# Optimization experiments

Measured on AMD Instinct MI355X. Metric: run time of the kernel, lower is better.

The kernel has to match this reference:

```python
import jax, jax.numpy as jnp
import numpy as np

N, E = 10000, 160000
MUL0, MUL1, MUL2 = 64, 32, 16
DIM = MUL0 + MUL1 * 3 + MUL2 * 5          # 240
LAT, CPL, NTYPE = 128, 128, 95
NGATE = MUL1 + MUL2                        # 48 gate scalars
NCH = MUL0 + MUL1 + MUL2                   # 112 irrep channels
AVG_NEI = 16.0

# scaling_indices: per-channel index repeated over each irrep's dim
SCALE_IDX = np.concatenate([
    np.arange(MUL0),
    np.repeat(np.arange(MUL0, MUL0 + MUL1), 3),
    np.repeat(np.arange(MUL0 + MUL1, NCH), 5),
])


def _split(x, n):
    s = x[:, :MUL0]
    v1 = x[:, MUL0:MUL0 + MUL1 * 3].reshape(n, MUL1, 3)
    v2 = x[:, MUL0 + MUL1 * 3:].reshape(n, MUL2, 5)
    return s, v1, v2


def setup_inputs() -> dict:
    key = jax.random.key(0)
    ks = iter(jax.random.split(key, 48))
    rn = lambda *s: jax.random.normal(next(ks), s, dtype=jnp.float32)
    return dict(
        node_features=rn(N, DIM), edge_features=rn(E, DIM),
        latents=rn(E, LAT), msg_cpl=rn(N, CPL),
        node_onehot=jax.random.uniform(next(ks), (N, NTYPE), dtype=jnp.float32),
        wigner_D1=rn(E, 3, 3), wigner_D2=rn(E, 5, 5),
        so2_W0=rn(2 * MUL0, MUL0 + NGATE) * 0.08, so2_W1=rn(2 * MUL1, MUL1) * 0.12,
        so2_W2=rn(2 * MUL2, MUL2) * 0.17, so2_Ws=rn(LAT, NCH + NGATE) * 0.08,
        env_W=rn(LAT, NCH) * 0.08,
        post_W0=rn(MUL0, MUL0) * 0.12, post_b0=rn(MUL0) * 0.01,
        post_W1=rn(MUL1, MUL1) * 0.17, post_W2=rn(MUL2, MUL2) * 0.25,
        res_W0=rn(MUL0, MUL0) * 0.12, res_b0=rn(MUL0) * 0.01,
        res_W1=rn(MUL1, MUL1) * 0.17, res_W2=rn(MUL2, MUL2) * 0.25,
        cpl_W1=rn(CPL, CPL) * 0.08, cpl_b1=rn(CPL) * 0.01,
        cpl_W2=rn(CPL, NCH) * 0.08, cpl_b2=rn(NCH) * 0.01,
        gs_W=rn(MUL0, CPL) * 0.12, gs_b=rn(CPL) * 0.01,
        msg_W1=rn(2 * CPL, CPL) * 0.06, msg_b1=rn(CPL) * 0.01,
        msg_W2=rn(CPL, CPL) * 0.08, msg_b2=rn(CPL) * 0.01,
        ln_g=jnp.ones(CPL, jnp.float32), ln_b=jnp.zeros(CPL, jnp.float32),
        oh_w0=rn(MUL0, NTYPE) * 0.1, oh_w1=rn(MUL1, NTYPE) * 0.1, oh_w2=rn(MUL2, NTYPE) * 0.1,
        edge_index=jax.random.randint(next(ks), (2, E), 0, N),
    )


def _forward(node_features, edge_features, latents, msg_cpl, node_onehot,
             wigner_D1, wigner_D2, so2_W0, so2_W1, so2_W2, so2_Ws, env_W,
             post_W0, post_b0, post_W1, post_W2, res_W0, res_b0, res_W1, res_W2,
             cpl_W1, cpl_b1, cpl_W2, cpl_b2, gs_W, gs_b,
             msg_W1, msg_b1, msg_W2, msg_b2, ln_g, ln_b,
             oh_w0, oh_w1, oh_w2, edge_index):
    src = edge_index[0]
    ns, nv1, nv2 = _split(node_features, N)
    es, ev1, ev2 = _split(edge_features, E)
    # gather node feats to edges, concat with edge feats (per-l blocks)
    s_in = jnp.concatenate([ns[src], es], axis=1)                 # [E,128]
    v1_in = jnp.concatenate([nv1[src], ev1], axis=1)              # [E,64,3]
    v2_in = jnp.concatenate([nv2[src], ev2], axis=1)              # [E,32,5]
    # rotate into per-edge frame (Wigner D)
    v1_r = jnp.einsum('eij,ecj->eci', wigner_D1, v1_in)
    v2_r = jnp.einsum('eij,ecj->eci', wigner_D2, v2_in)
    # SO2 linear: shared channel mixing + latent-conditioned per-channel scales
    sc = latents @ so2_Ws                                         # [E,160]
    s_m = (s_in @ so2_W0) * sc[:, :MUL0 + NGATE]
    v1_m = jnp.einsum('eci,co->eoi', v1_r, so2_W1) * sc[:, MUL0 + NGATE:MUL0 + NGATE + MUL1, None]
    v2_m = jnp.einsum('eci,co->eoi', v2_r, so2_W2) * sc[:, MUL0 + NGATE + MUL1:, None]
    # rotate back
    v1_m = jnp.einsum('eji,eci->ecj', wigner_D1, v1_m)
    v2_m = jnp.einsum('eji,eci->ecj', wigner_D2, v2_m)
    # Gate activation
    s_act = jax.nn.silu(s_m[:, :MUL0])
    gates = jax.nn.sigmoid(s_m[:, MUL0:])
    v1_g = v1_m * gates[:, :MUL1, None]
    v2_g = v2_m * gates[:, MUL1:, None]
    # lin_post (per-l linear, bias on scalars)
    s_p = s_act @ post_W0 + post_b0
    v1_p = jnp.einsum('eci,co->eoi', v1_g, post_W1)
    v2_p = jnp.einsum('eci,co->eoi', v2_g, post_W2)
    # env element-wise weighting from latents
    w = latents @ env_W                                           # [E,112]
    s_p = s_p * w[:, :MUL0]
    v1_p = v1_p * w[:, MUL0:MUL0 + MUL1, None]
    v2_p = v2_p * w[:, MUL0 + MUL1:, None]
    msg = jnp.concatenate([s_p, v1_p.reshape(E, -1), v2_p.reshape(E, -1)], axis=1)
    # scatter-reduce to nodes + neighbor normalization
    agg = jax.ops.segment_sum(msg, src, num_segments=N) * (AVG_NEI ** -0.5)
    # coupling coefficients (per-channel, expanded by scaling_indices)
    coeffs = jax.nn.silu(msg_cpl @ cpl_W1 + cpl_b1) @ cpl_W2 + cpl_b2
    new_nf = agg * coeffs[:, SCALE_IDX]
    # coupling-channel update
    scal = new_nf[:, :MUL0] @ gs_W + gs_b
    h = jnp.concatenate([scal, msg_cpl], axis=1)
    upd = jax.nn.silu(h @ msg_W1 + msg_b1) @ msg_W2 + msg_b2
    mc = msg_cpl + upd
    mu = mc.mean(-1, keepdims=True)
    var = mc.var(-1, keepdims=True)
    msg_cpl_out = (mc - mu) * jax.lax.rsqrt(var + 1e-5) * ln_g + ln_b
    # residual mix with fixed logit-0 coefficients
    c = jax.nn.sigmoid(jnp.float32(0.0))
    c_old = jax.lax.rsqrt(c * c + 1.0)
    c_new = c * c_old
    rs = ns @ res_W0 + res_b0
    rv1 = jnp.einsum('eci,co->eoi', nv1, res_W1)
    rv2 = jnp.einsum('eci,co->eoi', nv2, res_W2)
    res = jnp.concatenate([rs, rv1.reshape(N, -1), rv2.reshape(N, -1)], axis=1)
    nf = c_new * new_nf + c_old * res
    # layer one-hot tensor product ('uvu' with 95x0e)
    inv = 1.0 / np.sqrt(NTYPE).astype(np.float32)
    g0 = (node_onehot @ oh_w0.T) * inv
    g1 = (node_onehot @ oh_w1.T) * inv
    g2 = (node_onehot @ oh_w2.T) * inv
    os_, ov1, ov2 = _split(nf, N)
    oh = jnp.concatenate([os_ * g0, (ov1 * g1[:, :, None]).reshape(N, -1),
                          (ov2 * g2[:, :, None]).reshape(N, -1)], axis=1)
    return nf + oh, msg_cpl_out


def reference(node_features, edge_features, latents, msg_cpl, node_onehot,
              wigner_D1, wigner_D2, so2_W0, so2_W1, so2_W2, so2_Ws, env_W,
              post_W0, post_b0, post_W1, post_W2, res_W0, res_b0, res_W1, res_W2,
              cpl_W1, cpl_b1, cpl_W2, cpl_b2, gs_W, gs_b,
              msg_W1, msg_b1, msg_W2, msg_b2, ln_g, ln_b,
              oh_w0, oh_w1, oh_w2, edge_index):
    return _forward(node_features, edge_features, latents, msg_cpl, node_onehot,
                    wigner_D1, wigner_D2, so2_W0, so2_W1, so2_W2, so2_Ws, env_W,
                    post_W0, post_b0, post_W1, post_W2, res_W0, res_b0, res_W1, res_W2,
                    cpl_W1, cpl_b1, cpl_W2, cpl_b2, gs_W, gs_b,
                    msg_W1, msg_b1, msg_W2, msg_b2, ln_g, ln_b,
                    oh_w0, oh_w1, oh_w2, edge_index)
```

## Files before the change

kernel.cpp:

```cpp
#include <hip/hip_runtime.h>

#define NN   10000
#define NE   160000
#define DIM  240
#define EB   16
#define NPB  16

typedef __bf16 bf16x8 __attribute__((ext_vector_type(8)));
typedef __bf16 bf16x4 __attribute__((ext_vector_type(4)));
typedef float  f32x4  __attribute__((ext_vector_type(4)));

__device__ __forceinline__ float sigf(float x) { return 1.0f / (1.0f + __expf(-x)); }

#define OFF_WB1 0
#define OFF_WB2 34816
#define OFF_W1  49152
#define OFF_W2  51200
#define OFF_PW0 51712
#define OFF_PW1 55808
#define OFF_PW2 56832
#define OHT_BYTE_OFF 131072
#define CNT_BYTE_OFF 196608
#define ROW_BYTE_OFF 237568
#define CUR_BYTE_OFF 282624
#define EID_BYTE_OFF 327680

__global__ __launch_bounds__(256) void prep_kernel(
    const float* __restrict__ Ws, const float* __restrict__ We, const float* __restrict__ W0,
    const float* __restrict__ W1, const float* __restrict__ W2,
    const float* __restrict__ pW0, const float* __restrict__ pW1, const float* __restrict__ pW2,
    const float* __restrict__ w0g, const float* __restrict__ w1g, const float* __restrict__ w2g,
    __bf16* __restrict__ wsb, float* __restrict__ ohT,
    const int* __restrict__ src, int* __restrict__ cnt)
{
    if (blockIdx.x >= 56) {
        if (cnt) {
            int e = (blockIdx.x - 56) * 256 + threadIdx.x;
            if (e < NE) atomicAdd(&cnt[src[e]], 1);
        }
        return;
    }
    int tid = blockIdx.x * 256 + threadIdx.x;
    const int stride = 56 * 256;
    for (int idx = tid; idx < 17*4*512; idx += stride) {
        int j = idx & 7, lane = (idx >> 3) & 63, ks = (idx >> 9) & 3, nt = idx >> 11;
        int k = ks*32 + (lane >> 4)*8 + j, n = nt*16 + (lane & 15);
        float v = (n < 160) ? Ws[k*160 + n] : We[k*112 + (n - 160)];
        wsb[OFF_WB1 + idx] = (__bf16)v;
    }
    for (int idx = tid; idx < 7*4*512; idx += stride) {
        int j = idx & 7, lane = (idx >> 3) & 63, ks = (idx >> 9) & 3, nt = idx >> 11;
        int k = ks*32 + (lane >> 4)*8 + j, n = nt*16 + (lane & 15);
        wsb[OFF_WB2 + idx] = (__bf16)W0[k*112 + n];
    }
    for (int idx = tid; idx < 2*2*512; idx += stride) {
        int j = idx & 7, lane = (idx >> 3) & 63, ks = (idx >> 9) & 1, nt = idx >> 10;
        int k = ks*32 + (lane >> 4)*8 + j, n = nt*16 + (lane & 15);
        wsb[OFF_W1 + idx] = (__bf16)W1[k*32 + n];
    }
    for (int idx = tid; idx < 512; idx += stride) {
        int j = idx & 7, lane = (idx >> 3) & 63;
        int k = (lane >> 4)*8 + j, n = lane & 15;
        wsb[OFF_W2 + idx] = (__bf16)W2[k*16 + n];
    }
    for (int idx = tid; idx < 4*2*512; idx += stride) {
        int j = idx & 7, lane = (idx >> 3) & 63, ks = (idx >> 9) & 1, nt = idx >> 10;
        int k = ks*32 + (lane >> 4)*8 + j, n = nt*16 + (lane & 15);
        wsb[OFF_PW0 + idx] = (__bf16)pW0[k*64 + n];
    }
    for (int idx = tid; idx < 2*512; idx += stride) {
        int j = idx & 7, lane = (idx >> 3) & 63, nt = idx >> 9;
        int k = (lane >> 4)*8 + j, n = nt*16 + (lane & 15);
        wsb[OFF_PW1 + idx] = (__bf16)pW1[k*32 + n];
    }
    for (int idx = tid; idx < 512; idx += stride) {
        int j = idx & 7, lane = (idx >> 3) & 63;
        int k = (lane >> 4)*8 + j, n = lane & 15;
        wsb[OFF_PW2 + idx] = (k < 16) ? (__bf16)pW2[k*16 + n] : (__bf16)0.0f;
    }
    for (int idx = tid; idx < 96*112; idx += stride) {
        int k = idx / 112, n2 = idx - k*112;
        float v = 0.f;
        if (k < 95) {
            if (n2 < 64)      v = w0g[n2*95 + k];
            else if (n2 < 96) v = w1g[(n2-64)*95 + k];
            else              v = w2g[(n2-96)*95 + k];
        }
        ohT[idx] = v * 0.10259783521f;
    }
}

__global__ __launch_bounds__(256) void scan_kernel(const int* __restrict__ cnt,
                                                   int* __restrict__ rowptr, int* __restrict__ cur) {
    __shared__ int part[256];
    int t = threadIdx.x;
    int base = t * 40;
    int local[40];
    int s = 0;
    #pragma unroll
    for (int i = 0; i < 40; i++) {
        int idx = base + i;
        int v = (idx < NN) ? cnt[idx] : 0;
        local[i] = s; s += v;
    }
    part[t] = s;
    __syncthreads();
    for (int off = 1; off < 256; off <<= 1) {
        int v = (t >= off) ? part[t - off] : 0;
        __syncthreads();
        part[t] += v;
        __syncthreads();
    }
    int pre = (t > 0) ? part[t - 1] : 0;
    #pragma unroll
    for (int i = 0; i < 40; i++) {
        int idx = base + i;
        if (idx < NN) { int r = pre + local[i]; rowptr[idx] = r; cur[idx] = r; }
    }
    if (t == 255) rowptr[NN] = part[255];
}

__global__ __launch_bounds__(256) void fill_kernel(const int* __restrict__ src,
                                                   int* __restrict__ cur, int* __restrict__ eidl) {
    int e = blockIdx.x * 256 + threadIdx.x;
    if (e < NE) {
        int slot = atomicAdd(&cur[src[e]], 1);
        eidl[slot] = e;
    }
}

__global__ __launch_bounds__(256, 4) void edge_mfma_kernel(
    const float* __restrict__ nf, const float* __restrict__ ef,
    const float* __restrict__ latg, const float* __restrict__ D1g, const float* __restrict__ D2g,
    const float* __restrict__ pb0, const int* __restrict__ srcg,
    const int* __restrict__ eidl, const __bf16* __restrict__ wsb, float* agg)
{
    __shared__ __align__(16) unsigned char pool[40064];
    __bf16* Cb   = (__bf16*)(pool + 0);
    __bf16* aLat = (__bf16*)(pool + 12544);
    __bf16* aSin = (__bf16*)(pool + 16640);
    __bf16* v1m  = (__bf16*)(pool + 12544);
    __bf16* v2m  = (__bf16*)(pool + 16384);
    __bf16* mtile= (__bf16*)(pool + 12544);
    __bf16* vt1  = (__bf16*)(pool + 20736);
    __bf16* vt2  = (__bf16*)(pool + 27136);
    __bf16* aV1g = (__bf16*)(pool + 20736);
    __bf16* aV2g = (__bf16*)(pool + 23808);
    float*  d1s  = (float*)(pool + 32512);
    float*  d2s  = (float*)(pool + 33088);
    float*  gts  = (float*)(pool + 32512);
    __bf16* aSact= (__bf16*)(pool + 35648);
    float*  e1s  = (float*)(pool + 37696);
    float*  e2s  = (float*)(pool + 38272);
    int*    srcs = (int*)  (pool + 39872);
    int*    eids = (int*)  (pool + 39936);

    const int t    = threadIdx.x;
    const int wid  = t >> 6, lane = t & 63;
    const int e0   = blockIdx.x * EB;

    #define EIDX(e) (eidl ? eidl[e0 + (e)] : (e0 + (e)))

    bf16x8 bpre[8];
    {
        const __bf16* b0 = wsb + OFF_WB1 + wid*2048;
        const __bf16* b1 = wsb + OFF_WB1 + (wid + 4)*2048;
        #pragma unroll
        for (int ks = 0; ks < 4; ks++) {
            bpre[ks]     = *(const bf16x8*)(b0 + (ks*64 + lane)*8);
            bpre[4 + ks] = *(const bf16x8*)(b1 + (ks*64 + lane)*8);
        }
    }

    if (t < 16) { int ee = EIDX(t); eids[t] = ee; srcs[t] = srcg[ee]; }

    for (int idx = t; idx < 144; idx += 256) {
        int e = idx / 9; int ee = EIDX(e);
        d1s[idx] = D1g[(size_t)ee*9 + (idx - e*9)];
    }
    for (int idx = t; idx < 400; idx += 256) {
        int e = idx / 25; int ee = EIDX(e);
        d2s[idx] = D2g[(size_t)ee*25 + (idx - e*25)];
    }
    {
        int e = t >> 4, half = (t >> 3) & 1, cq = t & 7;
        int ee = EIDX(e);
        const float* base = half ? (ef + (size_t)ee*240 + 64 + cq*12)
                                 : (nf + (size_t)srcg[ee]*240 + 64 + cq*12);
        float4 f0 = *(const float4*)base;
        float4 f1 = *(const float4*)(base + 4);
        float4 f2 = *(const float4*)(base + 8);
        float f[12] = {f0.x,f0.y,f0.z,f0.w,f1.x,f1.y,f1.z,f1.w,f2.x,f2.y,f2.z,f2.w};
        int c = half*32 + cq*4;
        __bf16* dst = vt1 + e*200 + c;
        #pragma unroll
        for (int i = 0; i < 3; i++) {
            bf16x4 v = {(__bf16)f[i], (__bf16)f[3+i], (__bf16)f[6+i], (__bf16)f[9+i]};
            *(bf16x4*)(dst + i*64) = v;
        }
    }
    if (t < 128) {
        int e = t >> 3, half = (t >> 2) & 1, cq = t & 3;
        int ee = EIDX(e);
        const float* base = half ? (ef + (size_t)ee*240 + 160 + cq*20)
                                 : (nf + (size_t)srcg[ee]*240 + 160 + cq*20);
        float f[20];
        #pragma unroll
        for (int k = 0; k < 5; k++) {
            float4 q4 = *(const float4*)(base + k*4);
            f[4*k] = q4.x; f[4*k+1] = q4.y; f[4*k+2] = q4.z; f[4*k+3] = q4.w;
        }
        int c = half*16 + cq*4;
        __bf16* dst = vt2 + e*168 + c;
        #pragma unroll
        for (int z = 0; z < 5; z++) {
            bf16x4 v = {(__bf16)f[z], (__bf16)f[5+z], (__bf16)f[10+z], (__bf16)f[15+z]};
            *(bf16x4*)(dst + z*32) = v;
        }
    }
    {
        int ks = t >> 6, l2 = t & 63, e = l2 & 15;
        int k0 = ks*32 + (l2 >> 4)*8;
        int ee = EIDX(e);
        {
            const float4* p4 = (const float4*)(latg + (size_t)ee*128 + k0);
            float4 f0 = p4[0], f1 = p4[1];
            bf16x8 v;
            v[0]=(__bf16)f0.x; v[1]=(__bf16)f0.y; v[2]=(__bf16)f0.z; v[3]=(__bf16)f0.w;
            v[4]=(__bf16)f1.x; v[5]=(__bf16)f1.y; v[6]=(__bf16)f1.z; v[7]=(__bf16)f1.w;
            *(bf16x8*)(aLat + t*8) = v;
        }
        {
            const float* s2 = (k0 < 64) ? (nf + (size_t)srcg[ee]*240 + k0)
                                        : (ef + (size_t)ee*240 + (k0 - 64));
            const float4* p4 = (const float4*)s2;
            float4 f0 = p4[0], f1 = p4[1];
            bf16x8 v;
            v[0]=(__bf16)f0.x; v[1]=(__bf16)f0.y; v[2]=(__bf16)f0.z; v[3]=(__bf16)f0.w;
            v[4]=(__bf16)f1.x; v[5]=(__bf16)f1.y; v[6]=(__bf16)f1.z; v[7]=(__bf16)f1.w;
            *(bf16x8*)(aSin + t*8) = v;
        }
    }
    __syncthreads();

    {
        int col16 = lane & 15, ebase = (lane >> 4)*4;
        bf16x8 aL[4], aS[4];
        #pragma unroll
        for (int ks = 0; ks < 4; ks++) {
            aL[ks] = *(const bf16x8*)(aLat + (ks*64 + lane)*8);
            aS[ks] = *(const bf16x8*)(aSin + (ks*64 + lane)*8);
        }
        #pragma unroll
        for (int it = 0; it < 6; it++) {
            int nt = wid + it*4;
            bool isLat = nt < 17;
            const __bf16* bB = isLat ? (wsb + OFF_WB1 + nt*2048)
                                     : (wsb + OFF_WB2 + (nt - 17)*2048);
            f32x4 acc = {0.f, 0.f, 0.f, 0.f};
            #pragma unroll
            for (int ks = 0; ks < 4; ks++) {
                bf16x8 b;
                if (it < 2) b = bpre[it*4 + ks];
                else        b = *(const bf16x8*)(bB + (ks*64 + lane)*8);
                acc = __builtin_amdgcn_mfma_f32_16x16x32_bf16(isLat ? aL[ks] : aS[ks], b, acc, 0, 0, 0);
            }
            int col = (isLat ? nt*16 : 272 + (nt - 17)*16) + col16;
            #pragma unroll
            for (int r = 0; r < 4; r++) Cb[(ebase + r)*392 + col] = (__bf16)acc[r];
        }
    }
    for (int idx = t; idx < 544; idx += 256) {
        if (idx < 144) {
            int e = idx / 9, r = idx - e*9, i = r / 3, k = r - i*3;
            const float* d = d1s + e*9;
            e1s[idx] = d[i*3+0]*d[0*3+k] + d[i*3+1]*d[1*3+k] + d[i*3+2]*d[2*3+k];
        } else {
            int j = idx - 144;
            int e = j / 25, r = j - e*25, i = r / 5, k = r - i*5;
            const float* d = d2s + e*25;
            float a = 0.f;
            #pragma unroll
            for (int tt = 0; tt < 5; tt++) a += d[i*5+tt] * d[tt*5+k];
            e2s[j] = a;
        }
    }
    __syncthreads();

    {
        int col16 = lane & 15, er = lane & 15, q8 = (lane >> 4)*8, ebase = (lane >> 4)*4;
        for (int p = wid; p < 11; p += 4) {
            f32x4 acc = {0.f, 0.f, 0.f, 0.f};
            if (p < 6) {
                int i = p >> 1, nt = p & 1;
                #pragma unroll
                for (int ks = 0; ks < 2; ks++) {
                    bf16x8 a = *(const bf16x8*)(vt1 + er*200 + i*64 + ks*32 + q8);
                    bf16x8 b = *(const bf16x8*)(wsb + OFF_W1 + ((nt*2 + ks)*64 + lane)*8);
                    acc = __builtin_amdgcn_mfma_f32_16x16x32_bf16(a, b, acc, 0, 0, 0);
                }
                int col = nt*16 + col16;
                #pragma unroll
                for (int r = 0; r < 4; r++) v1m[(i*16 + ebase + r)*40 + col] = (__bf16)acc[r];
            } else {
                int i = p - 6;
                bf16x8 a = *(const bf16x8*)(vt2 + er*168 + i*32 + q8);
                bf16x8 b = *(const bf16x8*)(wsb + OFF_W2 + lane*8);
                acc = __builtin_amdgcn_mfma_f32_16x16x32_bf16(a, b, acc, 0, 0, 0);
                #pragma unroll
                for (int r = 0; r < 4; r++) v2m[(i*16 + ebase + r)*24 + col16] = (__bf16)acc[r];
            }
        }
    }
    if (t < 128) {
        int ks = t >> 6, l2 = t & 63, e = l2 & 15, o0 = ks*32 + (l2 >> 4)*8;
        bf16x8 v;
        #pragma unroll
        for (int j = 0; j < 8; j++) {
            int o = o0 + j;
            float x = (float)Cb[e*392 + 272 + o] * (float)Cb[e*392 + o];
            v[j] = (__bf16)(x * sigf(x));
        }
        *(bf16x8*)(aSact + t*8) = v;
    }
    for (int idx = t; idx < 768; idx += 256) {
        int e = idx / 48, o = idx - e*48;
        float x = (float)Cb[e*392 + 336 + o] * (float)Cb[e*392 + 64 + o];
        gts[e*49 + o] = sigf(x);
    }
    __syncthreads();

    for (int idx = t; idx < 512; idx += 256) {
        if (idx < 192) {
            int i = idx >> 6, l2 = idx & 63, e = l2 & 15, c0 = (l2 >> 4)*8;
            float z0 = e1s[e*9 + i*3], z1 = e1s[e*9 + i*3 + 1], z2 = e1s[e*9 + i*3 + 2];
            bf16x8 m0 = *(const bf16x8*)(v1m + (0*16 + e)*40 + c0);
            bf16x8 m1 = *(const bf16x8*)(v1m + (1*16 + e)*40 + c0);
            bf16x8 m2 = *(const bf16x8*)(v1m + (2*16 + e)*40 + c0);
            bf16x8 s8 = *(const bf16x8*)(Cb + e*392 + 112 + c0);
            bf16x8 v;
            #pragma unroll
            for (int j = 0; j < 8; j++) {
                float g = gts[e*49 + c0 + j];
                float a = z0*(float)m0[j] + z1*(float)m1[j] + z2*(float)m2[j];
                v[j] = (__bf16)(g * (float)s8[j] * a);
            }
            *(bf16x8*)(aV1g + idx*8) = v;
        } else {
            int idx2 = idx - 192;
            int i = idx2 >> 6, l2 = idx2 & 63, e = l2 & 15, c0 = (l2 >> 4)*8;
            bf16x8 v;
            if (c0 < 16) {
                const float* ee = e2s + e*25 + i*5;
                float z0 = ee[0], z1 = ee[1], z2 = ee[2], z3 = ee[3], z4 = ee[4];
                bf16x8 m0 = *(const bf16x8*)(v2m + (0*16 + e)*24 + c0);
                bf16x8 m1 = *(const bf16x8*)(v2m + (1*16 + e)*24 + c0);
                bf16x8 m2 = *(const bf16x8*)(v2m + (2*16 + e)*24 + c0);
                bf16x8 m3 = *(const bf16x8*)(v2m + (3*16 + e)*24 + c0);
                bf16x8 m4 = *(const bf16x8*)(v2m + (4*16 + e)*24 + c0);
                bf16x8 s8 = *(const bf16x8*)(Cb + e*392 + 144 + c0);
                #pragma unroll
                for (int j = 0; j < 8; j++) {
                    float g = gts[e*49 + 32 + c0 + j];
                    float a = z0*(float)m0[j] + z1*(float)m1[j] + z2*(float)m2[j]
                            + z3*(float)m3[j] + z4*(float)m4[j];
                    v[j] = (__bf16)(g * (float)s8[j] * a);
                }
            } else {
                #pragma unroll
                for (int j = 0; j < 8; j++) v[j] = (__bf16)0.0f;
            }
            *(bf16x8*)(aV2g + idx2*8) = v;
        }
    }
    __syncthreads();

    {
        int col16 = lane & 15, ebase = (lane >> 4)*4;
        for (int p = wid; p < 15; p += 4) {
            f32x4 acc = {0.f, 0.f, 0.f, 0.f};
            if (p < 4) {
                int nt = p;
                #pragma unroll
                for (int ks = 0; ks < 2; ks++) {
                    bf16x8 a = *(const bf16x8*)(aSact + (ks*64 + lane)*8);
                    bf16x8 b = *(const bf16x8*)(wsb + OFF_PW0 + ((nt*2 + ks)*64 + lane)*8);
                    acc = __builtin_amdgcn_mfma_f32_16x16x32_bf16(a, b, acc, 0, 0, 0);
                }
                int o = nt*16 + col16;
                float bias = pb0[o];
                #pragma unroll
                for (int r = 0; r < 4; r++) {
                    int e = ebase + r;
                    float val = (acc[r] + bias) * (float)Cb[e*392 + 160 + o];
                    if (eidl) mtile[e*248 + o] = (__bf16)val;
                    else      atomicAdd(agg + (size_t)srcs[e]*240 + o, val);
                }
            } else if (p < 10) {
                int q = p - 4, i = q >> 1, nt = q & 1;
                bf16x8 a = *(const bf16x8*)(aV1g + (i*64 + lane)*8);
                bf16x8 b = *(const bf16x8*)(wsb + OFF_PW1 + (nt*64 + lane)*8);
                acc = __builtin_amdgcn_mfma_f32_16x16x32_bf16(a, b, acc, 0, 0, 0);
                int o = nt*16 + col16;
                #pragma unroll
                for (int r = 0; r < 4; r++) {
                    int e = ebase + r;
                    float val = acc[r] * (float)Cb[e*392 + 224 + o];
                    if (eidl) mtile[e*248 + 64 + o*3 + i] = (__bf16)val;
                    else      atomicAdd(agg + (size_t)srcs[e]*240 + 64 + o*3 + i, val);
                }
            } else {
                int i = p - 10;
                bf16x8 a = *(const bf16x8*)(aV2g + (i*64 + lane)*8);
                bf16x8 b = *(const bf16x8*)(wsb + OFF_PW2 + lane*8);
                acc = __builtin_amdgcn_mfma_f32_16x16x32_bf16(a, b, acc, 0, 0, 0);
                #pragma unroll
                for (int r = 0; r < 4; r++) {
                    int e = ebase + r;
                    float val = acc[r] * (float)Cb[e*392 + 256 + col16];
                    if (eidl) mtile[e*248 + 160 + col16*5 + i] = (__bf16)val;
                    else      atomicAdd(agg + (size_t)srcs[e]*240 + 160 + col16*5 + i, val);
                }
            }
        }
    }

    if (eidl) {
        __syncthreads();
        if (t < 240) {
            float s = 0.f;
            int prev = srcs[0];
            #pragma unroll
            for (int e = 0; e < EB; e++) {
                int sn = srcs[e];
                if (sn != prev) {
                    atomicAdd(agg + (size_t)prev*240 + t, s);
                    s = 0.f; prev = sn;
                }
                s += (float)mtile[e*248 + t];
            }
            atomicAdd(agg + (size_t)prev*240 + t, s);
        }
    }
    #undef EIDX
}

__global__ __launch_bounds__(256, 2) void node_kernel(
    const float* __restrict__ nf, const float* __restrict__ mcplg,
    const float* __restrict__ ohg,
    const float* __restrict__ cW1, const float* __restrict__ cb1,
    const float* __restrict__ cW2, const float* __restrict__ cb2,
    const float* __restrict__ gsW, const float* __restrict__ gsb,
    const float* __restrict__ mW1, const float* __restrict__ mb1,
    const float* __restrict__ mW2, const float* __restrict__ mb2,
    const float* __restrict__ lng, const float* __restrict__ lnb,
    const float* __restrict__ rW0, const float* __restrict__ rb0,
    const float* __restrict__ rW1, const float* __restrict__ rW2,
    const float* __restrict__ ohT, float* out0, float* out1)
{
    __shared__ __align__(16) unsigned char pool[68608];
    float* mcp  = (float*)(pool + 0);
    float* ohv  = (float*)(pool + 8192);
    float* nsr  = (float*)(pool + 14336);
    float* anew = (float*)(pool + 29696);
    float* t12  = (float*)(pool + 45056);
    float* cfg  = (float*)(pool + 53248);
    float* scm  = (float*)(pool + 60416);

    const int t  = threadIdx.x;
    const int g  = t >> 7;
    const int o  = t & 127;
    const int nb = g * 8;
    const int n0 = blockIdx.x * NPB;

    for (int idx = t; idx < NPB * 128; idx += 256) {
        int n = idx >> 7, k = idx & 127;
        mcp[n*128 + k] = mcplg[(n0 + n) * 128 + k];
    }
    for (int idx = t; idx < NPB * 96; idx += 256) {
        int n = idx / 96, k = idx - n * 96;
        ohv[n*96 + k] = (k < 95) ? ohg[(n0 + n) * 95 + k] : 0.f;
    }
    for (int idx = t; idx < NPB * 240; idx += 256) {
        int n = idx / 240, k = idx - n * 240;
        nsr[n*240 + k]  = nf[(n0 + n) * DIM + k];
        anew[n*240 + k] = out0[(n0 + n) * DIM + k];
    }
    __syncthreads();

    {
        float a[8]; float b = cb1[o];
        #pragma unroll
        for (int i = 0; i < 8; i++) a[i] = b;
        #pragma unroll 2
        for (int k4 = 0; k4 < 32; k4++) {
            float w0 = cW1[(4*k4+0)*128 + o], w1 = cW1[(4*k4+1)*128 + o],
                  w2 = cW1[(4*k4+2)*128 + o], w3 = cW1[(4*k4+3)*128 + o];
            #pragma unroll
            for (int i = 0; i < 8; i++) {
                float4 m = *(const float4*)&mcp[(nb+i)*128 + 4*k4];
                a[i] += m.x*w0 + m.y*w1 + m.z*w2 + m.w*w3;
            }
        }
        #pragma unroll
        for (int i = 0; i < 8; i++) { float x = a[i]; t12[(nb+i)*128 + o] = x * sigf(x); }
    }
    __syncthreads();

    if (o < 112) {
        float a[8]; float b = cb2[o];
        #pragma unroll
        for (int i = 0; i < 8; i++) a[i] = b;
        #pragma unroll 2
        for (int k4 = 0; k4 < 32; k4++) {
            float w0 = cW2[(4*k4+0)*112 + o], w1 = cW2[(4*k4+1)*112 + o],
                  w2 = cW2[(4*k4+2)*112 + o], w3 = cW2[(4*k4+3)*112 + o];
            #pragma unroll
            for (int i = 0; i < 8; i++) {
                float4 m = *(const float4*)&t12[(nb+i)*128 + 4*k4];
                a[i] += m.x*w0 + m.y*w1 + m.z*w2 + m.w*w3;
            }
        }
        #pragma unroll
        for (int i = 0; i < 8; i++) cfg[(nb+i)*112 + o] = a[i];
    }
    __syncthreads();

    for (int idx = t; idx < NPB * 240; idx += 256) {
        int n = idx / 240, d = idx - n * 240;
        int ch = (d < 64) ? d : (d < 160 ? 64 + (d - 64) / 3 : 96 + (d - 160) / 5);
        anew[n*240 + d] *= 0.25f * cfg[n*112 + ch];
    }
    __syncthreads();

    {
        float a[8]; float b = gsb[o];
        #pragma unroll
        for (int i = 0; i < 8; i++) a[i] = b;
        #pragma unroll 2
        for (int k4 = 0; k4 < 16; k4++) {
            float w0 = gsW[(4*k4+0)*128 + o], w1 = gsW[(4*k4+1)*128 + o],
                  w2 = gsW[(4*k4+2)*128 + o], w3 = gsW[(4*k4+3)*128 + o];
            #pragma unroll
            for (int i = 0; i < 8; i++) {
                float4 m = *(const float4*)&anew[(nb+i)*240 + 4*k4];
                a[i] += m.x*w0 + m.y*w1 + m.z*w2 + m.w*w3;
            }
        }
        #pragma unroll
        for (int i = 0; i < 8; i++) scm[(nb+i)*128 + o] = a[i];
    }
    __syncthreads();

    {
        float a[8]; float b = mb1[o];
        #pragma unroll
        for (int i = 0; i < 8; i++) a[i] = b;
        #pragma unroll 2
        for (int k4 = 0; k4 < 32; k4++) {
            float w0 = mW1[(4*k4+0)*128 + o], w1 = mW1[(4*k4+1)*128 + o],
                  w2 = mW1[(4*k4+2)*128 + o], w3 = mW1[(4*k4+3)*128 + o];
            #pragma unroll
            for (int i = 0; i < 8; i++) {
                float4 m = *(const float4*)&scm[(nb+i)*128 + 4*k4];
                a[i] += m.x*w0 + m.y*w1 + m.z*w2 + m.w*w3;
            }
        }
        #pragma unroll 2
        for (int k4 = 0; k4 < 32; k4++) {
            float w0 = mW1[(128+4*k4+0)*128 + o], w1 = mW1[(128+4*k4+1)*128 + o],
                  w2 = mW1[(128+4*k4+2)*128 + o], w3 = mW1[(128+4*k4+3)*128 + o];
            #pragma unroll
            for (int i = 0; i < 8; i++) {
                float4 m = *(const float4*)&mcp[(nb+i)*128 + 4*k4];
                a[i] += m.x*w0 + m.y*w1 + m.z*w2 + m.w*w3;
            }
        }
        #pragma unroll
        for (int i = 0; i < 8; i++) { float x = a[i]; t12[(nb+i)*128 + o] = x * sigf(x); }
    }
    __syncthreads();

    {
        float a[8]; float b = mb2[o];
        #pragma unroll
        for (int i = 0; i < 8; i++) a[i] = b;
        #pragma unroll 2
        for (int k4 = 0; k4 < 32; k4++) {
            float w0 = mW2[(4*k4+0)*128 + o], w1 = mW2[(4*k4+1)*128 + o],
                  w2 = mW2[(4*k4+2)*128 + o], w3 = mW2[(4*k4+3)*128 + o];
            #pragma unroll
            for (int i = 0; i < 8; i++) {
                float4 m = *(const float4*)&t12[(nb+i)*128 + 4*k4];
                a[i] += m.x*w0 + m.y*w1 + m.z*w2 + m.w*w3;
            }
        }
        #pragma unroll
        for (int i = 0; i < 8; i++) scm[(nb+i)*128 + o] = mcp[(nb+i)*128 + o] + a[i];
    }
    __syncthreads();

    {
        int n = t >> 4, l = t & 15;
        float x[8]; float s = 0.f, ss = 0.f;
        #pragma unroll
        for (int i = 0; i < 8; i++) { x[i] = scm[n*128 + l + 16*i]; s += x[i]; ss += x[i]*x[i]; }
        #pragma unroll
        for (int off = 8; off > 0; off >>= 1) {
            s  += __shfl_down(s,  off, 16);
            ss += __shfl_down(ss, off, 16);
        }
        s  = __shfl(s, 0, 16);
        ss = __shfl(ss, 0, 16);
        float mu   = s * (1.f / 128.f);
        float var  = ss * (1.f / 128.f) - mu * mu;
        float rstd = rsqrtf(var + 1e-5f);
        float* op = out1 + (n0 + n) * 128;
        #pragma unroll
        for (int i = 0; i < 8; i++) {
            int c = l + 16*i;
            op[c] = (x[i] - mu) * rstd * lng[c] + lnb[c];
        }
    }

    if (o < 112) {
        float a[8] = {0.f,0.f,0.f,0.f,0.f,0.f,0.f,0.f};
        #pragma unroll 2
        for (int k4 = 0; k4 < 24; k4++) {
            float w0 = ohT[(4*k4+0)*112 + o], w1 = ohT[(4*k4+1)*112 + o],
                  w2 = ohT[(4*k4+2)*112 + o], w3 = ohT[(4*k4+3)*112 + o];
            #pragma unroll
            for (int i = 0; i < 8; i++) {
                float4 m = *(const float4*)&ohv[(nb+i)*96 + 4*k4];
                a[i] += m.x*w0 + m.y*w1 + m.z*w2 + m.w*w3;
            }
        }
        #pragma unroll
        for (int i = 0; i < 8; i++) cfg[(nb+i)*112 + o] = a[i];
    }
    __syncthreads();

    const float c_new = 0.4472135955f;
    const float c_old = 0.8944271910f;
    for (int idx = t; idx < NPB * 240; idx += 256) {
        int n = idx / 240, d = idx - n * 240;
        float res, gg;
        if (d < 64) {
            float acc = rb0[d];
            #pragma unroll 4
            for (int c = 0; c < 64; c++) acc += nsr[n*240 + c] * rW0[c * 64 + d];
            res = acc; gg = cfg[n*112 + d];
        } else if (d < 160) {
            int dd = d - 64, oo = dd / 3, j = dd - oo * 3;
            float acc = 0.f;
            #pragma unroll 4
            for (int c = 0; c < 32; c++) acc += nsr[n*240 + 64 + c*3 + j] * rW1[c * 32 + oo];
            res = acc; gg = cfg[n*112 + 64 + oo];
        } else {
            int dd = d - 160, oo = dd / 5, j = dd - oo * 5;
            float acc = 0.f;
            #pragma unroll 4
            for (int c = 0; c < 16; c++) acc += nsr[n*240 + 160 + c*5 + j] * rW2[c * 16 + oo];
            res = acc; gg = cfg[n*112 + 96 + oo];
        }
        float v = c_new * anew[n*240 + d] + c_old * res;
        out0[(n0 + n) * DIM + d] = v * (1.f + gg);
    }
}

extern "C" void kernel_launch(void* const* d_in, const int* in_sizes, int n_in,
                              void* d_out, int out_size, void* d_ws, size_t ws_size,
                              hipStream_t stream) {
    const float* nf      = (const float*)d_in[0];
    const float* ef      = (const float*)d_in[1];
    const float* lat     = (const float*)d_in[2];
    const float* mcpl    = (const float*)d_in[3];
    const float* ohot    = (const float*)d_in[4];
    const float* D1      = (const float*)d_in[5];
    const float* D2      = (const float*)d_in[6];
    const float* so2_W0  = (const float*)d_in[7];
    const float* so2_W1  = (const float*)d_in[8];
    const float* so2_W2  = (const float*)d_in[9];
    const float* so2_Ws  = (const float*)d_in[10];
    const float* env_W   = (const float*)d_in[11];
    const float* post_W0 = (const float*)d_in[12];
    const float* post_b0 = (const float*)d_in[13];
    const float* post_W1 = (const float*)d_in[14];
    const float* post_W2 = (const float*)d_in[15];
    const float* res_W0  = (const float*)d_in[16];
    const float* res_b0  = (const float*)d_in[17];
    const float* res_W1  = (const float*)d_in[18];
    const float* res_W2  = (const float*)d_in[19];
    const float* cpl_W1  = (const float*)d_in[20];
    const float* cpl_b1  = (const float*)d_in[21];
    const float* cpl_W2  = (const float*)d_in[22];
    const float* cpl_b2  = (const float*)d_in[23];
    const float* gs_W    = (const float*)d_in[24];
    const float* gs_b    = (const float*)d_in[25];
    const float* msg_W1  = (const float*)d_in[26];
    const float* msg_b1  = (const float*)d_in[27];
    const float* msg_W2  = (const float*)d_in[28];
    const float* msg_b2  = (const float*)d_in[29];
    const float* ln_g    = (const float*)d_in[30];
    const float* ln_b    = (const float*)d_in[31];
    const float* oh_w0   = (const float*)d_in[32];
    const float* oh_w1   = (const float*)d_in[33];
    const float* oh_w2   = (const float*)d_in[34];
    const int*   eidx    = (const int*)d_in[35];

    float* out0 = (float*)d_out;
    float* out1 = (float*)d_out + (size_t)NN * DIM;
    char*   wsB = (char*)d_ws;
    __bf16* wsb = (__bf16*)d_ws;
    float*  ohT = (float*)(wsB + OHT_BYTE_OFF);

    const size_t needA = (size_t)EID_BYTE_OFF + (size_t)NE * sizeof(int);
    const bool planA = ws_size >= needA;

    (void)hipMemsetAsync(out0, 0, (size_t)NN * DIM * sizeof(float), stream);

    if (planA) {
        int* cnt  = (int*)(wsB + CNT_BYTE_OFF);
        int* row  = (int*)(wsB + ROW_BYTE_OFF);
        int* cur  = (int*)(wsB + CUR_BYTE_OFF);
        int* eidl = (int*)(wsB + EID_BYTE_OFF);

        (void)hipMemsetAsync(cnt, 0, 10240 * sizeof(int), stream);
        prep_kernel<<<56 + (NE + 255) / 256, 256, 0, stream>>>(
            so2_Ws, env_W, so2_W0, so2_W1, so2_W2, post_W0, post_W1, post_W2,
            oh_w0, oh_w1, oh_w2, wsb, ohT, eidx, cnt);
        scan_kernel<<<1, 256, 0, stream>>>(cnt, row, cur);
        fill_kernel<<<(NE + 255) / 256, 256, 0, stream>>>(eidx, cur, eidl);

        edge_mfma_kernel<<<NE / EB, 256, 0, stream>>>(
            nf, ef, lat, D1, D2, post_b0, eidx, eidl, wsb, out0);
    } else {
        prep_kernel<<<56, 256, 0, stream>>>(
            so2_Ws, env_W, so2_W0, so2_W1, so2_W2, post_W0, post_W1, post_W2,
            oh_w0, oh_w1, oh_w2, wsb, ohT, eidx, nullptr);
        edge_mfma_kernel<<<NE / EB, 256, 0, stream>>>(
            nf, ef, lat, D1, D2, post_b0, eidx, nullptr, wsb, out0);
    }

    node_kernel<<<NN / NPB, 256, 0, stream>>>(
        nf, mcpl, ohot, cpl_W1, cpl_b1, cpl_W2, cpl_b2, gs_W, gs_b,
        msg_W1, msg_b1, msg_W2, msg_b2, ln_g, ln_b,
        res_W0, res_b0, res_W1, res_W2, ohT, out0, out1);
}
```

Before: 695.3 us.

## Load MFMA A-operands directly to registers, fuse gate sigmoid, shrink LDS footprints

In the edge kernel, latent and scalar inputs now go straight from global memory into MFMA A-operand registers instead of being staged through LDS. This removes one barrier and the preloaded B-fragment registers. The vector MFMAs and SiLU activation move before the next barrier, and the separate gate-sigmoid stage is folded into its consumer, dropping the gts buffer and another barrier. In the node kernel, the node-feature shared copy is removed and read from global memory instead, cutting LDS so the occupancy hint can go from 2 to 3 blocks. The cost is redundant global/cache reads and repeated sigmoid computation.

```diff
diff --git a/kernel.cpp b/kernel.cpp
--- a/kernel.cpp
+++ b/kernel.cpp
@@ -135,10 +135,8 @@
     const float* __restrict__ pb0, const int* __restrict__ srcg,
     const int* __restrict__ eidl, const __bf16* __restrict__ wsb, float* agg)
 {
-    __shared__ __align__(16) unsigned char pool[40064];
+    __shared__ __align__(16) unsigned char pool[39936];
     __bf16* Cb   = (__bf16*)(pool + 0);
-    __bf16* aLat = (__bf16*)(pool + 12544);
-    __bf16* aSin = (__bf16*)(pool + 16640);
     __bf16* v1m  = (__bf16*)(pool + 12544);
     __bf16* v2m  = (__bf16*)(pool + 16384);
     __bf16* mtile= (__bf16*)(pool + 12544);
@@ -148,12 +146,10 @@
     __bf16* aV2g = (__bf16*)(pool + 23808);
     float*  d1s  = (float*)(pool + 32512);
     float*  d2s  = (float*)(pool + 33088);
-    float*  gts  = (float*)(pool + 32512);
     __bf16* aSact= (__bf16*)(pool + 35648);
     float*  e1s  = (float*)(pool + 37696);
     float*  e2s  = (float*)(pool + 38272);
     int*    srcs = (int*)  (pool + 39872);
-    int*    eids = (int*)  (pool + 39936);
 
     const int t    = threadIdx.x;
     const int wid  = t >> 6, lane = t & 63;
@@ -161,18 +157,7 @@
 
     #define EIDX(e) (eidl ? eidl[e0 + (e)] : (e0 + (e)))
 
-    bf16x8 bpre[8];
-    {
-        const __bf16* b0 = wsb + OFF_WB1 + wid*2048;
-        const __bf16* b1 = wsb + OFF_WB1 + (wid + 4)*2048;
-        #pragma unroll
-        for (int ks = 0; ks < 4; ks++) {
-            bpre[ks]     = *(const bf16x8*)(b0 + (ks*64 + lane)*8);
-            bpre[4 + ks] = *(const bf16x8*)(b1 + (ks*64 + lane)*8);
-        }
-    }
-
-    if (t < 16) { int ee = EIDX(t); eids[t] = ee; srcs[t] = srcg[ee]; }
+    if (t < 16) srcs[t] = srcg[EIDX(t)];
 
     for (int idx = t; idx < 144; idx += 256) {
         int e = idx / 9; int ee = EIDX(e);
@@ -218,38 +203,30 @@
             *(bf16x4*)(dst + z*32) = v;
         }
     }
-    {
-        int ks = t >> 6, l2 = t & 63, e = l2 & 15;
-        int k0 = ks*32 + (l2 >> 4)*8;
-        int ee = EIDX(e);
-        {
-            const float4* p4 = (const float4*)(latg + (size_t)ee*128 + k0);
-            float4 f0 = p4[0], f1 = p4[1];
+
+    {
+        int col16 = lane & 15, ebase = (lane >> 4)*4;
+        int e = lane & 15, q = lane >> 4;
+        int ee = EIDX(e); int sn = srcg[ee];
+        const float* latp = latg + (size_t)ee*128 + q*8;
+        const float* nfp  = nf  + (size_t)sn*240 + q*8;
+        const float* efp  = ef  + (size_t)ee*240 + q*8;
+        bf16x8 aL[4], aS[4];
+        #pragma unroll
+        for (int ks = 0; ks < 4; ks++) {
+            float4 f0 = *(const float4*)(latp + ks*32);
+            float4 f1 = *(const float4*)(latp + ks*32 + 4);
             bf16x8 v;
             v[0]=(__bf16)f0.x; v[1]=(__bf16)f0.y; v[2]=(__bf16)f0.z; v[3]=(__bf16)f0.w;
             v[4]=(__bf16)f1.x; v[5]=(__bf16)f1.y; v[6]=(__bf16)f1.z; v[7]=(__bf16)f1.w;
-            *(bf16x8*)(aLat + t*8) = v;
-        }
-        {
-            const float* s2 = (k0 < 64) ? (nf + (size_t)srcg[ee]*240 + k0)
-                                        : (ef + (size_t)ee*240 + (k0 - 64));
-            const float4* p4 = (const float4*)s2;
-            float4 f0 = p4[0], f1 = p4[1];
-            bf16x8 v;
-            v[0]=(__bf16)f0.x; v[1]=(__bf16)f0.y; v[2]=(__bf16)f0.z; v[3]=(__bf16)f0.w;
-            v[4]=(__bf16)f1.x; v[5]=(__bf16)f1.y; v[6]=(__bf16)f1.z; v[7]=(__bf16)f1.w;
-            *(bf16x8*)(aSin + t*8) = v;
-        }
-    }
-    __syncthreads();
-
-    {
-        int col16 = lane & 15, ebase = (lane >> 4)*4;
-        bf16x8 aL[4], aS[4];
-        #pragma unroll
-        for (int ks = 0; ks < 4; ks++) {
-            aL[ks] = *(const bf16x8*)(aLat + (ks*64 + lane)*8);
-            aS[ks] = *(const bf16x8*)(aSin + (ks*64 + lane)*8);
+            aL[ks] = v;
+            const float* sp = (ks < 2) ? (nfp + ks*32) : (efp + (ks - 2)*32);
+            float4 g0 = *(const float4*)sp;
+            float4 g1 = *(const float4*)(sp + 4);
+            bf16x8 w;
+            w[0]=(__bf16)g0.x; w[1]=(__bf16)g0.y; w[2]=(__bf16)g0.z; w[3]=(__bf16)g0.w;
+            w[4]=(__bf16)g1.x; w[5]=(__bf16)g1.y; w[6]=(__bf16)g1.z; w[7]=(__bf16)g1.w;
+            aS[ks] = w;
         }
         #pragma unroll
         for (int it = 0; it < 6; it++) {
@@ -260,15 +237,51 @@
             f32x4 acc = {0.f, 0.f, 0.f, 0.f};
             #pragma unroll
             for (int ks = 0; ks < 4; ks++) {
-                bf16x8 b;
-                if (it < 2) b = bpre[it*4 + ks];
-                else        b = *(const bf16x8*)(bB + (ks*64 + lane)*8);
+                bf16x8 b = *(const bf16x8*)(bB + (ks*64 + lane)*8);
                 acc = __builtin_amdgcn_mfma_f32_16x16x32_bf16(isLat ? aL[ks] : aS[ks], b, acc, 0, 0, 0);
             }
             int col = (isLat ? nt*16 : 272 + (nt - 17)*16) + col16;
             #pragma unroll
             for (int r = 0; r < 4; r++) Cb[(ebase + r)*392 + col] = (__bf16)acc[r];
         }
+    }
+    __syncthreads();
+
+    {
+        int col16 = lane & 15, er = lane & 15, q8 = (lane >> 4)*8, ebase = (lane >> 4)*4;
+        for (int p = wid; p < 11; p += 4) {
+            f32x4 acc = {0.f, 0.f, 0.f, 0.f};
+            if (p < 6) {
+                int i = p >> 1, nt = p & 1;
+                #pragma unroll
+                for (int ks = 0; ks < 2; ks++) {
+                    bf16x8 a = *(const bf16x8*)(vt1 + er*200 + i*64 + ks*32 + q8);
+                    bf16x8 b = *(const bf16x8*)(wsb + OFF_W1 + ((nt*2 + ks)*64 + lane)*8);
+                    acc = __builtin_amdgcn_mfma_f32_16x16x32_bf16(a, b, acc, 0, 0, 0);
+                }
+                int col = nt*16 + col16;
+                #pragma unroll
+                for (int r = 0; r < 4; r++) v1m[(i*16 + ebase + r)*40 + col] = (__bf16)acc[r];
+            } else {
+                int i = p - 6;
+                bf16x8 a = *(const bf16x8*)(vt2 + er*168 + i*32 + q8);
+                bf16x8 b = *(const bf16x8*)(wsb + OFF_W2 + lane*8);
+                acc = __builtin_amdgcn_mfma_f32_16x16x32_bf16(a, b, acc, 0, 0, 0);
+                #pragma unroll
+                for (int r = 0; r < 4; r++) v2m[(i*16 + ebase + r)*24 + col16] = (__bf16)acc[r];
+            }
+        }
+    }
+    if (t < 128) {
+        int ks = t >> 6, l2 = t & 63, e = l2 & 15, o0 = ks*32 + (l2 >> 4)*8;
+        bf16x8 v;
+        #pragma unroll
+        for (int j = 0; j < 8; j++) {
+            int o = o0 + j;
+            float x = (float)Cb[e*392 + 272 + o] * (float)Cb[e*392 + o];
+            v[j] = (__bf16)(x * sigf(x));
+        }
+        *(bf16x8*)(aSact + t*8) = v;
     }
     for (int idx = t; idx < 544; idx += 256) {
         if (idx < 144) {
@@ -287,49 +300,6 @@
     }
     __syncthreads();
 
-    {
-        int col16 = lane & 15, er = lane & 15, q8 = (lane >> 4)*8, ebase = (lane >> 4)*4;
-        for (int p = wid; p < 11; p += 4) {
-            f32x4 acc = {0.f, 0.f, 0.f, 0.f};
-            if (p < 6) {
-                int i = p >> 1, nt = p & 1;
-                #pragma unroll
-                for (int ks = 0; ks < 2; ks++) {
-                    bf16x8 a = *(const bf16x8*)(vt1 + er*200 + i*64 + ks*32 + q8);
-                    bf16x8 b = *(const bf16x8*)(wsb + OFF_W1 + ((nt*2 + ks)*64 + lane)*8);
-                    acc = __builtin_amdgcn_mfma_f32_16x16x32_bf16(a, b, acc, 0, 0, 0);
-                }
-                int col = nt*16 + col16;
-                #pragma unroll
-                for (int r = 0; r < 4; r++) v1m[(i*16 + ebase + r)*40 + col] = (__bf16)acc[r];
-            } else {
-                int i = p - 6;
-                bf16x8 a = *(const bf16x8*)(vt2 + er*168 + i*32 + q8);
-                bf16x8 b = *(const bf16x8*)(wsb + OFF_W2 + lane*8);
-                acc = __builtin_amdgcn_mfma_f32_16x16x32_bf16(a, b, acc, 0, 0, 0);
-                #pragma unroll
-                for (int r = 0; r < 4; r++) v2m[(i*16 + ebase + r)*24 + col16] = (__bf16)acc[r];
-            }
-        }
-    }
-    if (t < 128) {
-        int ks = t >> 6, l2 = t & 63, e = l2 & 15, o0 = ks*32 + (l2 >> 4)*8;
-        bf16x8 v;
-        #pragma unroll
-        for (int j = 0; j < 8; j++) {
-            int o = o0 + j;
-            float x = (float)Cb[e*392 + 272 + o] * (float)Cb[e*392 + o];
-            v[j] = (__bf16)(x * sigf(x));
-        }
-        *(bf16x8*)(aSact + t*8) = v;
-    }
-    for (int idx = t; idx < 768; idx += 256) {
-        int e = idx / 48, o = idx - e*48;
-        float x = (float)Cb[e*392 + 336 + o] * (float)Cb[e*392 + 64 + o];
-        gts[e*49 + o] = sigf(x);
-    }
-    __syncthreads();
-
     for (int idx = t; idx < 512; idx += 256) {
         if (idx < 192) {
             int i = idx >> 6, l2 = idx & 63, e = l2 & 15, c0 = (l2 >> 4)*8;
@@ -338,10 +308,12 @@
             bf16x8 m1 = *(const bf16x8*)(v1m + (1*16 + e)*40 + c0);
             bf16x8 m2 = *(const bf16x8*)(v1m + (2*16 + e)*40 + c0);
             bf16x8 s8 = *(const bf16x8*)(Cb + e*392 + 112 + c0);
+            bf16x8 gA = *(const bf16x8*)(Cb + e*392 + 336 + c0);
+            bf16x8 gB = *(const bf16x8*)(Cb + e*392 + 64 + c0);
             bf16x8 v;
             #pragma unroll
             for (int j = 0; j < 8; j++) {
-                float g = gts[e*49 + c0 + j];
+                float g = sigf((float)gA[j] * (float)gB[j]);
                 float a = z0*(float)m0[j] + z1*(float)m1[j] + z2*(float)m2[j];
                 v[j] = (__bf16)(g * (float)s8[j] * a);
             }
@@ -359,9 +331,11 @@
                 bf16x8 m3 = *(const bf16x8*)(v2m + (3*16 + e)*24 + c0);
                 bf16x8 m4 = *(const bf16x8*)(v2m + (4*16 + e)*24 + c0);
                 bf16x8 s8 = *(const bf16x8*)(Cb + e*392 + 144 + c0);
+                bf16x8 gA = *(const bf16x8*)(Cb + e*392 + 368 + c0);
+                bf16x8 gB = *(const bf16x8*)(Cb + e*392 + 96 + c0);
                 #pragma unroll
                 for (int j = 0; j < 8; j++) {
-                    float g = gts[e*49 + 32 + c0 + j];
+                    float g = sigf((float)gA[j] * (float)gB[j]);
                     float a = z0*(float)m0[j] + z1*(float)m1[j] + z2*(float)m2[j]
                             + z3*(float)m3[j] + z4*(float)m4[j];
                     v[j] = (__bf16)(g * (float)s8[j] * a);
@@ -445,7 +419,7 @@
     #undef EIDX
 }
 
-__global__ __launch_bounds__(256, 2) void node_kernel(
+__global__ __launch_bounds__(256, 3) void node_kernel(
     const float* __restrict__ nf, const float* __restrict__ mcplg,
     const float* __restrict__ ohg,
     const float* __restrict__ cW1, const float* __restrict__ cb1,
@@ -458,14 +432,13 @@
     const float* __restrict__ rW1, const float* __restrict__ rW2,
     const float* __restrict__ ohT, float* out0, float* out1)
 {
-    __shared__ __align__(16) unsigned char pool[68608];
+    __shared__ __align__(16) unsigned char pool[53248];
     float* mcp  = (float*)(pool + 0);
     float* ohv  = (float*)(pool + 8192);
-    float* nsr  = (float*)(pool + 14336);
-    float* anew = (float*)(pool + 29696);
-    float* t12  = (float*)(pool + 45056);
-    float* cfg  = (float*)(pool + 53248);
-    float* scm  = (float*)(pool + 60416);
+    float* anew = (float*)(pool + 14336);
+    float* t12  = (float*)(pool + 29696);
+    float* cfg  = (float*)(pool + 37888);
+    float* scm  = (float*)(pool + 45056);
 
     const int t  = threadIdx.x;
     const int g  = t >> 7;
@@ -483,7 +456,6 @@
     }
     for (int idx = t; idx < NPB * 240; idx += 256) {
         int n = idx / 240, k = idx - n * 240;
-        nsr[n*240 + k]  = nf[(n0 + n) * DIM + k];
         anew[n*240 + k] = out0[(n0 + n) * DIM + k];
     }
     __syncthreads();
@@ -644,23 +616,24 @@
     const float c_old = 0.8944271910f;
     for (int idx = t; idx < NPB * 240; idx += 256) {
         int n = idx / 240, d = idx - n * 240;
+        const float* nrow = nf + (size_t)(n0 + n) * DIM;
         float res, gg;
         if (d < 64) {
             float acc = rb0[d];
             #pragma unroll 4
-            for (int c = 0; c < 64; c++) acc += nsr[n*240 + c] * rW0[c * 64 + d];
+            for (int c = 0; c < 64; c++) acc += nrow[c] * rW0[c * 64 + d];
             res = acc; gg = cfg[n*112 + d];
         } else if (d < 160) {
             int dd = d - 64, oo = dd / 3, j = dd - oo * 3;
             float acc = 0.f;
             #pragma unroll 4
-            for (int c = 0; c < 32; c++) acc += nsr[n*240 + 64 + c*3 + j] * rW1[c * 32 + oo];
+            for (int c = 0; c < 32; c++) acc += nrow[64 + c*3 + j] * rW1[c * 32 + oo];
             res = acc; gg = cfg[n*112 + 64 + oo];
         } else {
             int dd = d - 160, oo = dd / 5, j = dd - oo * 5;
             float acc = 0.f;
             #pragma unroll 4
-            for (int c = 0; c < 16; c++) acc += nsr[n*240 + 160 + c*5 + j] * rW2[c * 16 + oo];
+            for (int c = 0; c < 16; c++) acc += nrow[160 + c*5 + j] * rW2[c * 16 + oo];
             res = acc; gg = cfg[n*112 + 96 + oo];
         }
         float v = c_new * anew[n*240 + d] + c_old * res;
```

Measured after the change: 689.2 us. No clear change (-0.9%).
